# Kernel optimization log

Hardware: AMD Instinct MI355X
Metric: run time of the kernel (lower is better)

The kernel has to match this reference:

```python
import jax, jax.numpy as jnp
import numpy as np


def setup_inputs() -> dict:
    key = jax.random.key(0)
    k1, k2 = jax.random.split(key)
    B, L, D = 8, 4096, 1024
    hidden_states = jax.random.normal(k1, (B, L, D), dtype=jnp.float32)
    token_mask = jax.random.bernoulli(k2, 0.5, (B, L))
    return {"hidden_states": hidden_states, "token_mask": token_mask}


def reference(hidden_states, token_mask):
    """Compact hidden states at masked positions, left-packed and zero-padded.

    Returns (chunked: (B, M, D), counts: (B,)) where M = max tokens per row.
    Vectorized: prefix-sum over the mask gives per-row scatter destinations;
    masked-out positions are routed to a scratch slot M that is sliced off.
    """
    B, L, D = hidden_states.shape
    counts = token_mask.sum(axis=1).astype(jnp.int32)  # (B,)
    M = int(jnp.max(counts))  # data-dependent pad width (eager, matches .item())
    if M == 0:
        return hidden_states[:, :0, :], counts
    # destination index within each row: 0..count-1 for kept tokens, M for dropped
    dest = jnp.where(token_mask, jnp.cumsum(token_mask, axis=1) - 1, M)  # (B, L)
    b_idx = jnp.arange(B)[:, None]  # (B, 1)
    out = jnp.zeros((B, M + 1, D), hidden_states.dtype)
    out = out.at[b_idx, dest].set(hidden_states)  # single fused scatter
    chunked = out[:, :M, :]  # drop scratch slot
    return chunked, counts
```

## Files before the change

### kernel.cpp

```cpp
#include <hip/hip_runtime.h>


typedef float floatx4 __attribute__((ext_vector_type(4)));

__global__ __launch_bounds__(256) void fused_pack(
        const floatx4* __restrict__ hidden,
        const int*     __restrict__ mask,
        floatx4*       __restrict__ out,
        float*         __restrict__ counts_out,
        int L, int M, int D4, int nrows, int rpb) {
    __shared__ unsigned long long words[64];
    __shared__ int excl[65];

    const int t    = threadIdx.x;
    const int lane = t & 63;
    const int wid  = t >> 6;

    int r = blockIdx.x * rpb;
    const int r1 = min(nrows, r + rpb);
    if (r >= r1) return;

    while (r < r1) {
        const int b = r / M;
        const int mstart = r - b * M;
        const int mend   = min(r1 - b * M, M);

        const int* mrow = mask + (size_t)b * L;
        #pragma unroll
        for (int i = 0; i < 16; ++i) {
            const int k = wid * 16 + i;
            const unsigned long long bal = __ballot(mrow[k * 64 + lane] != 0);
            if (lane == 0) words[k] = bal;
        }
        __syncthreads();

        if (wid == 0) {
            const int pc = __popcll(words[lane]);
            int incl = pc;
            #pragma unroll
            for (int off = 1; off < 64; off <<= 1) {
                const int up = __shfl_up(incl, off, 64);
                if (lane >= off) incl += up;
            }
            excl[lane] = incl - pc;
            if (lane == 63) excl[64] = incl;
        }
        __syncthreads();

        const int cnt = excl[64];
        if (t == 0) counts_out[b] = (float)cnt;

        for (int m = mstart; m < mend; ++m, ++r) {
            const size_t orow = ((size_t)b * M + m) * D4;
            if (m < cnt) {
                int lo = 0, hi = 63;
                #pragma unroll
                for (int s = 0; s < 6; ++s) {
                    const int mid = (lo + hi + 1) >> 1;
                    if (excl[mid] <= m) lo = mid; else hi = mid - 1;
                }
                unsigned long long w = words[lo];
                const int j = m - excl[lo];
                for (int q = 0; q < j; ++q) w &= w - 1;
                const int l = lo * 64 + __builtin_ctzll(w);

                const size_t irow = ((size_t)b * L + l) * D4;
                for (int i = t; i < D4; i += 256) {
                    const floatx4 v = __builtin_nontemporal_load(&hidden[irow + i]);
                    __builtin_nontemporal_store(v, &out[orow + i]);
                }
            } else {
                const floatx4 z = (floatx4){0.f, 0.f, 0.f, 0.f};
                for (int i = t; i < D4; i += 256)
                    __builtin_nontemporal_store(z, &out[orow + i]);
            }
        }
        __syncthreads();
    }
}

__global__ void zero_counts(float* counts_out, int B) {
    if ((int)threadIdx.x < B) counts_out[threadIdx.x] = 0.f;
}

extern "C" void kernel_launch(void* const* d_in, const int* in_sizes, int n_in,
                              void* d_out, int out_size, void* d_ws, size_t ws_size,
                              hipStream_t stream) {
    const int B  = 8;
    const int BL = in_sizes[1];
    const int D  = in_sizes[0] / BL;
    const int L  = BL / B;
    const int M  = (out_size - B) / (B * D);

    const float* hidden = (const float*)d_in[0];
    const int*   mask   = (const int*)d_in[1];
    float*       out    = (float*)d_out;
    float* counts_out   = out + (size_t)B * M * D;

    if (M == 0) {
        zero_counts<<<1, 64, 0, stream>>>(counts_out, B);
        return;
    }

    const int nrows = B * M;
    const int rpb   = (nrows + 2047) / 2048;
    const int grid  = (nrows + rpb - 1) / rpb;
    fused_pack<<<grid, 256, 0, stream>>>((const floatx4*)hidden, mask,
                                         (floatx4*)out, counts_out,
                                         L, M, D / 4, nrows, rpb);
}
```

Before: 202.6 us.

## Process fixed 8-row groups per block with parallel source lookup and batched loads

Each block now handles up to 8 output rows from a single batch row. The source index for each output row is resolved in parallel by separate threads into shared memory, instead of serially per row. For D=1024 the kernel then issues all 8 row loads before any stores, putting more memory traffic in flight per thread. The cost is more blocks, and each block redoes the mask ballot and prefix scan, so mask reads and scan work increase.

```diff
diff --git a/kernel.cpp b/kernel.cpp
--- a/kernel.cpp
+++ b/kernel.cpp
@@ -2,80 +2,106 @@
 
 
 typedef float floatx4 __attribute__((ext_vector_type(4)));
+
+#define RPB 8
 
 __global__ __launch_bounds__(256) void fused_pack(
         const floatx4* __restrict__ hidden,
         const int*     __restrict__ mask,
         floatx4*       __restrict__ out,
         float*         __restrict__ counts_out,
-        int L, int M, int D4, int nrows, int rpb) {
+        int L, int M, int D4, int Nb) {
     __shared__ unsigned long long words[64];
     __shared__ int excl[65];
+    __shared__ int srcrow[RPB];
 
     const int t    = threadIdx.x;
     const int lane = t & 63;
     const int wid  = t >> 6;
 
-    int r = blockIdx.x * rpb;
-    const int r1 = min(nrows, r + rpb);
-    if (r >= r1) return;
+    const int g  = blockIdx.x;
+    const int b  = g / Nb;
+    const int bi = g - b * Nb;
+    const int m0 = bi * RPB;
+    const int nm = min(M - m0, RPB);
 
-    while (r < r1) {
-        const int b = r / M;
-        const int mstart = r - b * M;
-        const int mend   = min(r1 - b * M, M);
+    const int* mrow = mask + (size_t)b * L;
+    #pragma unroll
+    for (int i = 0; i < 16; ++i) {
+        const int k = wid * 16 + i;
+        const unsigned long long bal = __ballot(mrow[k * 64 + lane] != 0);
+        if (lane == 0) words[k] = bal;
+    }
+    __syncthreads();
 
-        const int* mrow = mask + (size_t)b * L;
+    if (wid == 0) {
+        const int pc = __popcll(words[lane]);
+        int incl = pc;
         #pragma unroll
-        for (int i = 0; i < 16; ++i) {
-            const int k = wid * 16 + i;
-            const unsigned long long bal = __ballot(mrow[k * 64 + lane] != 0);
-            if (lane == 0) words[k] = bal;
+        for (int off = 1; off < 64; off <<= 1) {
+            const int up = __shfl_up(incl, off, 64);
+            if (lane >= off) incl += up;
         }
-        __syncthreads();
+        excl[lane] = incl - pc;
+        if (lane == 63) excl[64] = incl;
+    }
+    __syncthreads();
 
-        if (wid == 0) {
-            const int pc = __popcll(words[lane]);
-            int incl = pc;
+    const int cnt = excl[64];
+    if (t == 0 && bi == 0) counts_out[b] = (float)cnt;
+
+    if (t < nm) {
+        const int m = m0 + t;
+        int s = -1;
+        if (m < cnt) {
+            int lo = 0, hi = 63;
             #pragma unroll
-            for (int off = 1; off < 64; off <<= 1) {
-                const int up = __shfl_up(incl, off, 64);
-                if (lane >= off) incl += up;
+            for (int st = 0; st < 6; ++st) {
+                const int mid = (lo + hi + 1) >> 1;
+                if (excl[mid] <= m) lo = mid; else hi = mid - 1;
             }
-            excl[lane] = incl - pc;
-            if (lane == 63) excl[64] = incl;
+            unsigned long long w = words[lo];
+            const int j = m - excl[lo];
+            for (int q = 0; q < j; ++q) w &= w - 1;
+            s = lo * 64 + __builtin_ctzll(w);
         }
-        __syncthreads();
+        srcrow[t] = s;
+    }
+    __syncthreads();
 
-        const int cnt = excl[64];
-        if (t == 0) counts_out[b] = (float)cnt;
+    const floatx4 z = (floatx4){0.f, 0.f, 0.f, 0.f};
 
-        for (int m = mstart; m < mend; ++m, ++r) {
-            const size_t orow = ((size_t)b * M + m) * D4;
-            if (m < cnt) {
-                int lo = 0, hi = 63;
-                #pragma unroll
-                for (int s = 0; s < 6; ++s) {
-                    const int mid = (lo + hi + 1) >> 1;
-                    if (excl[mid] <= m) lo = mid; else hi = mid - 1;
-                }
-                unsigned long long w = words[lo];
-                const int j = m - excl[lo];
-                for (int q = 0; q < j; ++q) w &= w - 1;
-                const int l = lo * 64 + __builtin_ctzll(w);
-
-                const size_t irow = ((size_t)b * L + l) * D4;
-                for (int i = t; i < D4; i += 256) {
-                    const floatx4 v = __builtin_nontemporal_load(&hidden[irow + i]);
-                    __builtin_nontemporal_store(v, &out[orow + i]);
-                }
+    if (D4 == 256) {
+        floatx4 v[RPB];
+        const size_t ibase = (size_t)b * L * 256;
+        #pragma unroll
+        for (int m = 0; m < RPB; ++m) {
+            if (m < nm) {
+                const int s = srcrow[m];
+                v[m] = (s >= 0)
+                    ? __builtin_nontemporal_load(&hidden[ibase + (size_t)s * 256 + t])
+                    : z;
+            }
+        }
+        const size_t obase = ((size_t)b * M + m0) * 256 + t;
+        #pragma unroll
+        for (int m = 0; m < RPB; ++m)
+            if (m < nm)
+                __builtin_nontemporal_store(v[m], &out[obase + (size_t)m * 256]);
+    } else {
+        for (int m = 0; m < nm; ++m) {
+            const int s = srcrow[m];
+            const size_t orow = ((size_t)b * M + m0 + m) * D4;
+            if (s >= 0) {
+                const size_t irow = ((size_t)b * L + s) * D4;
+                for (int i = t; i < D4; i += 256)
+                    __builtin_nontemporal_store(
+                        __builtin_nontemporal_load(&hidden[irow + i]), &out[orow + i]);
             } else {
-                const floatx4 z = (floatx4){0.f, 0.f, 0.f, 0.f};
                 for (int i = t; i < D4; i += 256)
                     __builtin_nontemporal_store(z, &out[orow + i]);
             }
         }
-        __syncthreads();
     }
 }
 
@@ -102,10 +128,9 @@
         return;
     }
 
-    const int nrows = B * M;
-    const int rpb   = (nrows + 2047) / 2048;
-    const int grid  = (nrows + rpb - 1) / rpb;
+    const int Nb   = (M + RPB - 1) / RPB;
+    const int grid = B * Nb;
     fused_pack<<<grid, 256, 0, stream>>>((const floatx4*)hidden, mask,
                                          (floatx4*)out, counts_out,
-                                         L, M, D / 4, nrows, rpb);
+                                         L, M, D / 4, Nb);
 }
```

New measurement: 220.1 us. +8.6%, slower.
